# Kernel tuning notes

Hardware: AMD Instinct MI355X
Metric: run time of the kernel (lower is better)

## Reference

```python
import jax, jax.numpy as jnp
import numpy as np

DIM = 64
K = 8
B_TAIL = 3.0
HIDDEN = 64
BATCH = 16384
MIN_BIN_WIDTH = 1e-3
MIN_BIN_HEIGHT = 1e-3
MIN_DERIVATIVE = 1e-3


def setup_inputs() -> dict:
    key = jax.random.key(0)
    ks = jax.random.split(key, 8)
    L = DIM - 1
    out_dim = 3 * K - 1
    def u(k, shape, fan_in):
        b = 1.0 / np.sqrt(fan_in)
        return jax.random.uniform(k, shape, minval=-b, maxval=b, dtype=jnp.float32)
    return {
        "x": jax.random.normal(ks[0], (BATCH, DIM), jnp.float32),
        "init_param": jax.random.uniform(ks[1], (out_dim,), minval=-0.5, maxval=0.5, dtype=jnp.float32),
        # conditioner MLP i (i=1..dim-1) maps x[:, :i] -> 3K-1; stacked with zero-masked inputs
        "W1": u(ks[2], (L, HIDDEN, DIM), DIM),
        "b1": u(ks[3], (L, HIDDEN), DIM),
        "W2": u(ks[4], (L, HIDDEN, HIDDEN), HIDDEN),
        "b2": u(ks[5], (L, HIDDEN), HIDDEN),
        "W3": u(ks[6], (L, out_dim, HIDDEN), HIDDEN),
        "b3": u(ks[7], (L, out_dim), HIDDEN),
    }


def _rqs(inputs, uW, uH, uD, left, right):
    # inputs: [D, B]; uW/uH: [D, B, K]; uD: [D, B, K+1] (already edge-padded)
    num_bins = uW.shape[-1]
    widths = jax.nn.softmax(uW, axis=-1)
    widths = MIN_BIN_WIDTH + (1 - MIN_BIN_WIDTH * num_bins) * widths
    cw = jnp.pad(jnp.cumsum(widths, axis=-1), ((0, 0), (0, 0), (1, 0)))
    cw = (right - left) * cw + left
    cw = cw.at[..., 0].set(left).at[..., -1].set(right)
    widths = cw[..., 1:] - cw[..., :-1]

    derivs = MIN_DERIVATIVE + jax.nn.softplus(uD)

    heights = jax.nn.softmax(uH, axis=-1)
    heights = MIN_BIN_HEIGHT + (1 - MIN_BIN_HEIGHT * num_bins) * heights
    ch = jnp.pad(jnp.cumsum(heights, axis=-1), ((0, 0), (0, 0), (1, 0)))
    ch = (right - left) * ch + left  # bottom=left, top=right (symmetric box)
    ch = ch.at[..., 0].set(left).at[..., -1].set(right)
    heights = ch[..., 1:] - ch[..., :-1]

    # searchsorted: sum(inputs >= bin_edges) - 1, with eps on last edge
    cw_s = cw.at[..., -1].add(1e-6)
    bin_idx = jnp.sum(inputs[..., None] >= cw_s, axis=-1) - 1
    bin_idx = jnp.clip(bin_idx, 0, num_bins - 1)[..., None]
    take = lambda a: jnp.take_along_axis(a, bin_idx, axis=-1)[..., 0]

    in_cw = take(cw)
    in_w = take(widths)
    in_ch = take(ch)
    in_h = take(heights)
    in_delta = take(heights / widths)
    d_k = take(derivs)
    d_k1 = take(derivs[..., 1:])

    theta = (inputs - in_cw) / in_w
    t1mt = theta * (1 - theta)
    numer = in_h * (in_delta * theta**2 + d_k * t1mt)
    denom = in_delta + (d_k + d_k1 - 2 * in_delta) * t1mt
    outputs = in_ch + numer / denom
    dnum = in_delta**2 * (d_k1 * theta**2 + 2 * in_delta * t1mt + d_k * (1 - theta) ** 2)
    logabsdet = jnp.log(dnum) - 2 * jnp.log(denom)
    return outputs, logabsdet


def _unconstrained_rqs(inputs, uW, uH, uD, tail_bound):
    inside = (inputs >= -tail_bound) & (inputs <= tail_bound)
    const = float(np.log(np.exp(1 - MIN_DERIVATIVE) - 1))
    uD = jnp.pad(uD, ((0, 0), (0, 0), (1, 1)), constant_values=const)
    x_in = jnp.clip(inputs, -tail_bound, tail_bound)
    out, ld = _rqs(x_in, uW, uH, uD, -tail_bound, tail_bound)
    return jnp.where(inside, out, inputs), jnp.where(inside, ld, 0.0)


def reference(x, init_param, W1, b1, W2, b2, W3, b3):
    Bsz = x.shape[0]
    L = DIM - 1
    # row l of mask keeps x[:, :l+1], zeroes the rest -> identical to per-layer x[:, :i]
    mask = jnp.tril(jnp.ones((L, DIM), x.dtype))
    xm = x[None, :, :] * mask[:, None, :]                         # [L, B, D]
    h = jnp.tanh(jnp.einsum('lbd,lhd->lbh', xm, W1) + b1[:, None, :])
    h = jnp.tanh(jnp.einsum('lbh,lgh->lbg', h, W2) + b2[:, None, :])
    out = jnp.einsum('lbh,loh->lbo', h, W3) + b3[:, None, :]      # [L, B, 3K-1]
    params = jnp.concatenate(
        [jnp.broadcast_to(init_param, (1, Bsz, 3 * K - 1)), out], axis=0)  # [D, B, 3K-1]
    W = 2 * B_TAIL * jax.nn.softmax(params[..., :K], axis=-1)
    H = 2 * B_TAIL * jax.nn.softmax(params[..., K:2 * K], axis=-1)
    Dp = jax.nn.softplus(params[..., 2 * K:])
    z_t, ld = _unconstrained_rqs(x.T, W, H, Dp, B_TAIL)           # [D, B]
    return z_t.T, ld.sum(axis=0)
```

## Files before the change

### kernel.cpp

```cpp
#include <hip/hip_runtime.h>

#define BATCH 16384
#define LAYERS 63
#define BM 128
#define XS 72
#define BLOB_BYTES 21504
#define LDS_OFF 8192
#define LDS_BYTES 13312

typedef float f4 __attribute__((ext_vector_type(4)));
typedef short s8 __attribute__((ext_vector_type(8)));
typedef unsigned int u4 __attribute__((ext_vector_type(4)));

__device__ __forceinline__ float rcpf(float v) { return __builtin_amdgcn_rcpf(v); }

__device__ __forceinline__ float fast_tanh(float v) {
    float e = __expf(2.f * v);
    return 1.f - 2.f * rcpf(e + 1.f);
}
__device__ __forceinline__ float softplus_f(float v) {
    return fmaxf(v, 0.f) + __logf(1.f + __expf(-fabsf(v)));
}
__device__ __forceinline__ unsigned short f2bf(float f) {
    unsigned int u = __float_as_uint(f);
    u += 0x7fffu + ((u >> 16) & 1u);
    return (unsigned short)(u >> 16);
}
#if __has_builtin(__builtin_amdgcn_cvt_pk_bf16_f32)
__device__ __forceinline__ unsigned pk2(float a, float b) {
    auto r = __builtin_amdgcn_cvt_pk_bf16_f32(a, b);
    return __builtin_bit_cast(unsigned, r);
}
#else
__device__ __forceinline__ unsigned pk2(float a, float b) {
    return (unsigned)f2bf(a) | ((unsigned)f2bf(b) << 16);
}
#endif
__device__ __forceinline__ unsigned long long pack4(float a, float b, float c, float d) {
    return (unsigned long long)pk2(a, b) | ((unsigned long long)pk2(c, d) << 32);
}

__device__ __forceinline__ void rqs_eval(const float* p, float xv, float& zout, float& ldout) {
    const bool inside = (xv >= -3.f) && (xv <= 3.f);
    const float xi = fminf(fmaxf(xv, -3.f), 3.f);

    float wa[8], ha[8];
    {
        float s = 0.f;
        #pragma unroll
        for (int i = 0; i < 8; i++) { wa[i] = __expf(p[i]); s += wa[i]; }
        float inv = 6.f * rcpf(s);
        #pragma unroll
        for (int i = 0; i < 8; i++) wa[i] *= inv;
        s = 0.f;
        #pragma unroll
        for (int i = 0; i < 8; i++) { wa[i] = __expf(wa[i]); s += wa[i]; }
        inv = 0.992f * rcpf(s);
        #pragma unroll
        for (int i = 0; i < 8; i++) wa[i] = 1e-3f + wa[i] * inv;
    }
    {
        float s = 0.f;
        #pragma unroll
        for (int i = 0; i < 8; i++) { ha[i] = __expf(p[8 + i]); s += ha[i]; }
        float inv = 6.f * rcpf(s);
        #pragma unroll
        for (int i = 0; i < 8; i++) ha[i] *= inv;
        s = 0.f;
        #pragma unroll
        for (int i = 0; i < 8; i++) { ha[i] = __expf(ha[i]); s += ha[i]; }
        inv = 0.992f * rcpf(s);
        #pragma unroll
        for (int i = 0; i < 8; i++) ha[i] = 1e-3f + ha[i] * inv;
    }

    float cw[9], ch[9];
    cw[0] = -3.f; ch[0] = -3.f;
    {
        float cs = 0.f, hs = 0.f;
        #pragma unroll
        for (int k = 1; k < 8; k++) {
            cs += wa[k - 1]; cw[k] = 6.f * cs - 3.f;
            hs += ha[k - 1]; ch[k] = 6.f * hs - 3.f;
        }
    }
    cw[8] = 3.f; ch[8] = 3.f;

    int cnt = 0;
    #pragma unroll
    for (int k = 0; k < 8; k++) cnt += (xi >= cw[k]) ? 1 : 0;
    cnt += (xi >= 3.000001f) ? 1 : 0;
    const int bin = min(max(cnt - 1, 0), 7);

    float in_cw = 0.f, in_w = 1.f, in_ch = 0.f, in_h = 1.f;
    float pd0 = 0.f, pd1 = 0.f;
    #pragma unroll
    for (int k = 0; k < 8; k++)
        if (k == bin) {
            in_cw = cw[k]; in_w = cw[k + 1] - cw[k];
            in_ch = ch[k]; in_h = ch[k + 1] - ch[k];
            if (k >= 1) pd0 = p[15 + k];
            if (k <= 6) pd1 = p[16 + k];
        }
    const float dk  = (bin == 0) ? 1.f : 1e-3f + softplus_f(softplus_f(pd0));
    const float dk1 = (bin == 7) ? 1.f : 1e-3f + softplus_f(softplus_f(pd1));

    const float rw    = rcpf(in_w);
    const float delta = in_h * rw;
    const float th    = (xi - in_cw) * rw;
    const float omt = 1.f - th;
    const float t1  = th * omt;
    const float th2 = th * th;
    const float numer = in_h * (delta * th2 + dk * t1);
    const float denom = delta + (dk + dk1 - 2.f * delta) * t1;
    const float outv  = in_ch + numer * rcpf(denom);
    const float dnum  = delta * delta * (dk1 * th2 + 2.f * delta * t1 + dk * omt * omt);
    const float ldv = __logf(dnum) - 2.f * __logf(denom);

    zout  = inside ? outv : xv;
    ldout = inside ? ldv : 0.f;
}

__global__ __launch_bounds__(256) void prep_kernel(
    const float* __restrict__ W1, const float* __restrict__ W2, const float* __restrict__ W3,
    const float* __restrict__ b1, const float* __restrict__ b2, const float* __restrict__ b3,
    unsigned char* __restrict__ blobG)
{
    const int tid = threadIdx.x;
    const int l = blockIdx.x;
    unsigned char* gb = blobG + (size_t)l * BLOB_BYTES;
    for (int e = tid; e < 1024; e += 256) {
        int m = e >> 9, r = (e >> 3) & 63, j = e & 7;
        const float* src = (m ? W2 : W1) + (size_t)l * 4096 + r * 64 + j * 8;
        unsigned long long lo = pack4(src[0], src[1], src[2], src[3]);
        unsigned long long hi = pack4(src[4], src[5], src[6], src[7]);
        unsigned long long* dst = (unsigned long long*)(gb + m * 8192 + r * 128 + ((j ^ (r & 7)) << 4));
        dst[0] = lo; dst[1] = hi;
    }
    if (tid < 256) {
        int r = tid >> 3, j = tid & 7;
        unsigned long long lo = 0ull, hi = 0ull;
        if (r < 23) {
            const float* src = W3 + (size_t)l * 1472 + r * 64 + j * 8;
            lo = pack4(src[0], src[1], src[2], src[3]);
            hi = pack4(src[4], src[5], src[6], src[7]);
        }
        unsigned long long* dst = (unsigned long long*)(gb + 16384 + r * 128 + ((j ^ (r & 7)) << 4));
        dst[0] = lo; dst[1] = hi;
    }
    if (tid < 64)        *(float*)(gb + 20480 + tid * 4)         = b1[l * 64 + tid];
    else if (tid < 128)  *(float*)(gb + 20736 + (tid - 64) * 4)  = b2[l * 64 + tid - 64];
    else if (tid < 160)  *(float*)(gb + 20992 + (tid - 128) * 4) = (tid - 128 < 23) ? b3[l * 23 + tid - 128] : 0.f;
    else                 { int e = tid - 160; if (e < 96) *(float*)(gb + 21120 + e * 4) = 0.f; }
}

__global__ __launch_bounds__(256, 5) void mlp_rqs_kernel(
    const float* __restrict__ x, const float* __restrict__ init_param,
    const unsigned char* __restrict__ blobG,
    float* __restrict__ z, float* __restrict__ ld)
{
    const int l = blockIdx.y;
    const int tid = threadIdx.x;

    if (l == LAYERS) {
        if (tid < 128) {
            const int row = blockIdx.x * 128 + tid;
            float p[23];
            #pragma unroll
            for (int j = 0; j < 23; j++) p[j] = init_param[j];
            float zv, lv;
            rqs_eval(p, x[(size_t)row * 64], zv, lv);
            z[(size_t)row * 64] = zv;
            unsafeAtomicAdd(ld + row, lv);
        }
        return;
    }

    const int keff = l + 1;
    const int b0 = blockIdx.x * BM;
    const int ln = tid & 63, wv = tid >> 6;
    const int c = ln & 15, q = ln >> 4;
    const int mbase = wv * 32;
    const int c7 = c & 7;

    __shared__ __align__(16) unsigned char blob[LDS_BYTES];
    __shared__ __align__(16) unsigned short Hs[BM * XS];

    unsigned short* W2s = (unsigned short*)blob;
    unsigned short* W3s = (unsigned short*)(blob + 8192);
    const float* b1s = (const float*)(blob + 12288);
    const float* b2s = (const float*)(blob + 12544);
    const float* b3s = (const float*)(blob + 12800);
    float* PsF = (float*)Hs;

    const unsigned char* gblob = blobG + (size_t)l * BLOB_BYTES;

    for (int t = wv; t < 13; t += 4)
        __builtin_amdgcn_global_load_lds(
            (const __attribute__((address_space(1))) void*)(gblob + LDS_OFF + t * 1024 + ln * 16),
            (__attribute__((address_space(3))) void*)(blob + t * 1024 + ln * 16), 16, 0, 0);

    const int ks1 = (keff + 31) >> 5;

    s8 aw1[2][4];
    #pragma unroll
    for (int mt = 0; mt < 4; mt++)
        aw1[0][mt] = *(const s8*)(gblob + (mt * 16 + c) * 128 + ((q ^ c7) << 4));
    if (ks1 == 2) {
        #pragma unroll
        for (int mt = 0; mt < 4; mt++)
            aw1[1][mt] = *(const s8*)(gblob + (mt * 16 + c) * 128 + (((4 + q) ^ c7) << 4));
    }

    u4 B0u, B1u, B2u{}, B3u{};
    {
        const float* xr = x + (size_t)(b0 + mbase + c) * 64 + q * 8;
        f4 v0a = *(const f4*)xr,            v0b = *(const f4*)(xr + 4);
        f4 v1a = *(const f4*)(xr + 1024),   v1b = *(const f4*)(xr + 1028);
        B0u = u4{pk2(v0a[0], v0a[1]), pk2(v0a[2], v0a[3]), pk2(v0b[0], v0b[1]), pk2(v0b[2], v0b[3])};
        B1u = u4{pk2(v1a[0], v1a[1]), pk2(v1a[2], v1a[3]), pk2(v1b[0], v1b[1]), pk2(v1b[2], v1b[3])};
        if (ks1 == 2) {
            f4 w0a = *(const f4*)(xr + 32),        w0b = *(const f4*)(xr + 36);
            f4 w1a = *(const f4*)(xr + 1024 + 32), w1b = *(const f4*)(xr + 1024 + 36);
            B2u = u4{pk2(w0a[0], w0a[1]), pk2(w0a[2], w0a[3]), pk2(w0b[0], w0b[1]), pk2(w0b[2], w0b[3])};
            B3u = u4{pk2(w1a[0], w1a[1]), pk2(w1a[2], w1a[3]), pk2(w1b[0], w1b[1]), pk2(w1b[2], w1b[3])};
        }
        const int n = keff - ((ks1 - 1) * 32 + q * 8);
        unsigned mk[4];
        #pragma unroll
        for (int i = 0; i < 4; i++) {
            int m = n - 2 * i;
            mk[i] = (m >= 2) ? 0xFFFFFFFFu : ((m == 1) ? 0xFFFFu : 0u);
        }
        if (ks1 == 2) {
            #pragma unroll
            for (int i = 0; i < 4; i++) { B2u[i] &= mk[i]; B3u[i] &= mk[i]; }
        } else {
            #pragma unroll
            for (int i = 0; i < 4; i++) { B0u[i] &= mk[i]; B1u[i] &= mk[i]; }
        }
    }
    const float xv = x[(size_t)(b0 + (tid & 127)) * 64 + keff];

    __syncthreads();

    {
        f4 acc[4][2];
        #pragma unroll
        for (int mt = 0; mt < 4; mt++) {
            f4 bv = *(const f4*)&b1s[mt * 16 + q * 4];
            acc[mt][0] = bv; acc[mt][1] = bv;
        }
        {
            s8 bx0 = __builtin_bit_cast(s8, B0u), bx1 = __builtin_bit_cast(s8, B1u);
            #pragma unroll
            for (int mt = 0; mt < 4; mt++) {
                acc[mt][0] = __builtin_amdgcn_mfma_f32_16x16x32_bf16(aw1[0][mt], bx0, acc[mt][0], 0, 0, 0);
                acc[mt][1] = __builtin_amdgcn_mfma_f32_16x16x32_bf16(aw1[0][mt], bx1, acc[mt][1], 0, 0, 0);
            }
        }
        if (ks1 == 2) {
            s8 bx0 = __builtin_bit_cast(s8, B2u), bx1 = __builtin_bit_cast(s8, B3u);
            #pragma unroll
            for (int mt = 0; mt < 4; mt++) {
                acc[mt][0] = __builtin_amdgcn_mfma_f32_16x16x32_bf16(aw1[1][mt], bx0, acc[mt][0], 0, 0, 0);
                acc[mt][1] = __builtin_amdgcn_mfma_f32_16x16x32_bf16(aw1[1][mt], bx1, acc[mt][1], 0, 0, 0);
            }
        }
        #pragma unroll
        for (int mt = 0; mt < 4; mt++)
            #pragma unroll
            for (int nt = 0; nt < 2; nt++) {
                f4 a = acc[mt][nt];
                unsigned long long w = (unsigned long long)pk2(fast_tanh(a[0]), fast_tanh(a[1]))
                    | ((unsigned long long)pk2(fast_tanh(a[2]), fast_tanh(a[3])) << 32);
                *(unsigned long long*)&Hs[(mbase + nt * 16 + c) * XS + mt * 16 + q * 4] = w;
            }
    }

    {
        f4 acc[4][2];
        #pragma unroll
        for (int mt = 0; mt < 4; mt++) {
            f4 bv = *(const f4*)&b2s[mt * 16 + q * 4];
            acc[mt][0] = bv; acc[mt][1] = bv;
        }
        #pragma unroll
        for (int ks = 0; ks < 2; ks++) {
            s8 bh0 = *(const s8*)&Hs[(mbase + c) * XS + ks * 32 + q * 8];
            s8 bh1 = *(const s8*)&Hs[(mbase + 16 + c) * XS + ks * 32 + q * 8];
            const int sb = ((ks * 4 + q) ^ c7) * 8;
            #pragma unroll
            for (int mt = 0; mt < 4; mt++) {
                s8 aw = *(const s8*)&W2s[(mt * 16 + c) * 64 + sb];
                acc[mt][0] = __builtin_amdgcn_mfma_f32_16x16x32_bf16(aw, bh0, acc[mt][0], 0, 0, 0);
                acc[mt][1] = __builtin_amdgcn_mfma_f32_16x16x32_bf16(aw, bh1, acc[mt][1], 0, 0, 0);
            }
        }
        #pragma unroll
        for (int mt = 0; mt < 4; mt++)
            #pragma unroll
            for (int nt = 0; nt < 2; nt++) {
                f4 a = acc[mt][nt];
                unsigned long long w = (unsigned long long)pk2(fast_tanh(a[0]), fast_tanh(a[1]))
                    | ((unsigned long long)pk2(fast_tanh(a[2]), fast_tanh(a[3])) << 32);
                *(unsigned long long*)&Hs[(mbase + nt * 16 + c) * XS + mt * 16 + q * 4] = w;
            }
    }

    {
        f4 acc3[2][2];
        #pragma unroll
        for (int mt = 0; mt < 2; mt++) {
            f4 bv = *(const f4*)&b3s[mt * 16 + q * 4];
            acc3[mt][0] = bv; acc3[mt][1] = bv;
        }
        #pragma unroll
        for (int ks = 0; ks < 2; ks++) {
            s8 bh0 = *(const s8*)&Hs[(mbase + c) * XS + ks * 32 + q * 8];
            s8 bh1 = *(const s8*)&Hs[(mbase + 16 + c) * XS + ks * 32 + q * 8];
            const int sb = ((ks * 4 + q) ^ c7) * 8;
            #pragma unroll
            for (int mt = 0; mt < 2; mt++) {
                s8 aw = *(const s8*)&W3s[(mt * 16 + c) * 64 + sb];
                acc3[mt][0] = __builtin_amdgcn_mfma_f32_16x16x32_bf16(aw, bh0, acc3[mt][0], 0, 0, 0);
                acc3[mt][1] = __builtin_amdgcn_mfma_f32_16x16x32_bf16(aw, bh1, acc3[mt][1], 0, 0, 0);
            }
        }
        #pragma unroll
        for (int mt = 0; mt < 2; mt++)
            #pragma unroll
            for (int nt = 0; nt < 2; nt++)
                *(f4*)&PsF[(mbase + nt * 16 + c) * 36 + mt * 16 + q * 4] = acc3[mt][nt];
    }
    __syncthreads();

    if (tid < BM) {
        float p[23];
        #pragma unroll
        for (int j = 0; j < 23; j++) p[j] = PsF[tid * 36 + j];
        float zv, lv;
        rqs_eval(p, xv, zv, lv);
        z[(size_t)(b0 + tid) * 64 + keff] = zv;
        unsafeAtomicAdd(ld + b0 + tid, lv);
    }
}

extern "C" void kernel_launch(void* const* d_in, const int* in_sizes, int n_in,
                              void* d_out, int out_size, void* d_ws, size_t ws_size,
                              hipStream_t stream)
{
    const float* x  = (const float*)d_in[0];
    const float* ip = (const float*)d_in[1];
    const float* W1 = (const float*)d_in[2];
    const float* b1 = (const float*)d_in[3];
    const float* W2 = (const float*)d_in[4];
    const float* b2 = (const float*)d_in[5];
    const float* W3 = (const float*)d_in[6];
    const float* b3 = (const float*)d_in[7];

    float* z  = (float*)d_out;
    float* ld = z + (size_t)BATCH * 64;

    unsigned char* blobG = (unsigned char*)d_ws;

    prep_kernel<<<LAYERS, 256, 0, stream>>>(W1, W2, W3, b1, b2, b3, blobG);
    hipMemsetAsync(ld, 0, BATCH * sizeof(float), stream);
    mlp_rqs_kernel<<<dim3(BATCH / BM, LAYERS + 1), 256, 0, stream>>>(
        x, ip, blobG, z, ld);
}
```

Before: 134.0 us.

## Shrink LDS footprint with swizzled H buffer and register-held W3 to raise occupancy

Replaces the padded H staging buffer (stride 72) with an unpadded XOR-swizzled layout and swizzles the parameter output buffer as well, so bank conflicts stay low without padding. W3 is no longer staged through LDS; each wave loads its fragments directly from global memory into registers. The blob layout is repacked so only W2 and the biases go to LDS, and launch bounds rise from 5 to 6 blocks per CU. The aim is more resident blocks per CU, traded against extra global loads for W3 and more register pressure.

```diff
diff --git a/kernel.cpp b/kernel.cpp
--- a/kernel.cpp
+++ b/kernel.cpp
@@ -3,10 +3,8 @@
 #define BATCH 16384
 #define LAYERS 63
 #define BM 128
-#define XS 72
 #define BLOB_BYTES 21504
-#define LDS_OFF 8192
-#define LDS_BYTES 13312
+#define LDSA_BYTES 9216
 
 typedef float f4 __attribute__((ext_vector_type(4)));
 typedef short s8 __attribute__((ext_vector_type(8)));
@@ -145,16 +143,16 @@
             lo = pack4(src[0], src[1], src[2], src[3]);
             hi = pack4(src[4], src[5], src[6], src[7]);
         }
-        unsigned long long* dst = (unsigned long long*)(gb + 16384 + r * 128 + ((j ^ (r & 7)) << 4));
+        unsigned long long* dst = (unsigned long long*)(gb + 17408 + r * 128 + ((j ^ (r & 7)) << 4));
         dst[0] = lo; dst[1] = hi;
     }
-    if (tid < 64)        *(float*)(gb + 20480 + tid * 4)         = b1[l * 64 + tid];
-    else if (tid < 128)  *(float*)(gb + 20736 + (tid - 64) * 4)  = b2[l * 64 + tid - 64];
-    else if (tid < 160)  *(float*)(gb + 20992 + (tid - 128) * 4) = (tid - 128 < 23) ? b3[l * 23 + tid - 128] : 0.f;
-    else                 { int e = tid - 160; if (e < 96) *(float*)(gb + 21120 + e * 4) = 0.f; }
-}
-
-__global__ __launch_bounds__(256, 5) void mlp_rqs_kernel(
+    if (tid < 64)        *(float*)(gb + 16384 + tid * 4)         = b1[l * 64 + tid];
+    else if (tid < 128)  *(float*)(gb + 16640 + (tid - 64) * 4)  = b2[l * 64 + tid - 64];
+    else if (tid < 160)  *(float*)(gb + 16896 + (tid - 128) * 4) = (tid - 128 < 23) ? b3[l * 23 + tid - 128] : 0.f;
+    else                 *(float*)(gb + 17024 + (tid - 160) * 4) = 0.f;
+}
+
+__global__ __launch_bounds__(256, 6) void mlp_rqs_kernel(
     const float* __restrict__ x, const float* __restrict__ init_param,
     const unsigned char* __restrict__ blobG,
     float* __restrict__ z, float* __restrict__ ld)
@@ -183,22 +181,21 @@
     const int mbase = wv * 32;
     const int c7 = c & 7;
 
-    __shared__ __align__(16) unsigned char blob[LDS_BYTES];
-    __shared__ __align__(16) unsigned short Hs[BM * XS];
-
-    unsigned short* W2s = (unsigned short*)blob;
-    unsigned short* W3s = (unsigned short*)(blob + 8192);
-    const float* b1s = (const float*)(blob + 12288);
-    const float* b2s = (const float*)(blob + 12544);
-    const float* b3s = (const float*)(blob + 12800);
+    __shared__ __align__(16) unsigned char ldsA[LDSA_BYTES];
+    __shared__ __align__(16) unsigned short Hs[BM * 64];
+
+    unsigned short* W2s = (unsigned short*)ldsA;
+    const float* b1s = (const float*)(ldsA + 8192);
+    const float* b2s = (const float*)(ldsA + 8448);
+    const float* b3s = (const float*)(ldsA + 8704);
     float* PsF = (float*)Hs;
 
     const unsigned char* gblob = blobG + (size_t)l * BLOB_BYTES;
 
-    for (int t = wv; t < 13; t += 4)
+    for (int t = wv; t < 9; t += 4)
         __builtin_amdgcn_global_load_lds(
-            (const __attribute__((address_space(1))) void*)(gblob + LDS_OFF + t * 1024 + ln * 16),
-            (__attribute__((address_space(3))) void*)(blob + t * 1024 + ln * 16), 16, 0, 0);
+            (const __attribute__((address_space(1))) void*)(gblob + 8192 + t * 1024 + ln * 16),
+            (__attribute__((address_space(3))) void*)(ldsA + t * 1024 + ln * 16), 16, 0, 0);
 
     const int ks1 = (keff + 31) >> 5;
 
@@ -242,6 +239,9 @@
     }
     const float xv = x[(size_t)(b0 + (tid & 127)) * 64 + keff];
 
+    const int row0 = (mbase + c) * 64, row1 = (mbase + 16 + c) * 64;
+    const int qoff = (q & 1) << 2, qhalf = q >> 1;
+
     __syncthreads();
 
     {
@@ -274,9 +274,17 @@
                 f4 a = acc[mt][nt];
                 unsigned long long w = (unsigned long long)pk2(fast_tanh(a[0]), fast_tanh(a[1]))
                     | ((unsigned long long)pk2(fast_tanh(a[2]), fast_tanh(a[3])) << 32);
-                *(unsigned long long*)&Hs[(mbase + nt * 16 + c) * XS + mt * 16 + q * 4] = w;
-            }
-    }
+                *(unsigned long long*)&Hs[(nt ? row1 : row0)
+                    + ((((mt << 1) + qhalf) ^ c7) << 3) + qoff] = w;
+            }
+    }
+
+    s8 aw3[2][2];
+    #pragma unroll
+    for (int ks = 0; ks < 2; ks++)
+        #pragma unroll
+        for (int mt = 0; mt < 2; mt++)
+            aw3[ks][mt] = *(const s8*)(gblob + 17408 + (mt * 16 + c) * 128 + (((ks * 4 + q) ^ c7) << 4));
 
     {
         f4 acc[4][2];
@@ -287,8 +295,8 @@
         }
         #pragma unroll
         for (int ks = 0; ks < 2; ks++) {
-            s8 bh0 = *(const s8*)&Hs[(mbase + c) * XS + ks * 32 + q * 8];
-            s8 bh1 = *(const s8*)&Hs[(mbase + 16 + c) * XS + ks * 32 + q * 8];
+            s8 bh0 = *(const s8*)&Hs[row0 + (((ks * 4 + q) ^ c7) << 3)];
+            s8 bh1 = *(const s8*)&Hs[row1 + (((ks * 4 + q) ^ c7) << 3)];
             const int sb = ((ks * 4 + q) ^ c7) * 8;
             #pragma unroll
             for (int mt = 0; mt < 4; mt++) {
@@ -304,7 +312,8 @@
                 f4 a = acc[mt][nt];
                 unsigned long long w = (unsigned long long)pk2(fast_tanh(a[0]), fast_tanh(a[1]))
                     | ((unsigned long long)pk2(fast_tanh(a[2]), fast_tanh(a[3])) << 32);
-                *(unsigned long long*)&Hs[(mbase + nt * 16 + c) * XS + mt * 16 + q * 4] = w;
+                *(unsigned long long*)&Hs[(nt ? row1 : row0)
+                    + ((((mt << 1) + qhalf) ^ c7) << 3) + qoff] = w;
             }
     }
 
@@ -317,28 +326,30 @@
         }
         #pragma unroll
         for (int ks = 0; ks < 2; ks++) {
-            s8 bh0 = *(const s8*)&Hs[(mbase + c) * XS + ks * 32 + q * 8];
-            s8 bh1 = *(const s8*)&Hs[(mbase + 16 + c) * XS + ks * 32 + q * 8];
-            const int sb = ((ks * 4 + q) ^ c7) * 8;
+            s8 bh0 = *(const s8*)&Hs[row0 + (((ks * 4 + q) ^ c7) << 3)];
+            s8 bh1 = *(const s8*)&Hs[row1 + (((ks * 4 + q) ^ c7) << 3)];
             #pragma unroll
             for (int mt = 0; mt < 2; mt++) {
-                s8 aw = *(const s8*)&W3s[(mt * 16 + c) * 64 + sb];
-                acc3[mt][0] = __builtin_amdgcn_mfma_f32_16x16x32_bf16(aw, bh0, acc3[mt][0], 0, 0, 0);
-                acc3[mt][1] = __builtin_amdgcn_mfma_f32_16x16x32_bf16(aw, bh1, acc3[mt][1], 0, 0, 0);
+                acc3[mt][0] = __builtin_amdgcn_mfma_f32_16x16x32_bf16(aw3[ks][mt], bh0, acc3[mt][0], 0, 0, 0);
+                acc3[mt][1] = __builtin_amdgcn_mfma_f32_16x16x32_bf16(aw3[ks][mt], bh1, acc3[mt][1], 0, 0, 0);
             }
         }
         #pragma unroll
         for (int mt = 0; mt < 2; mt++)
             #pragma unroll
             for (int nt = 0; nt < 2; nt++)
-                *(f4*)&PsF[(mbase + nt * 16 + c) * 36 + mt * 16 + q * 4] = acc3[mt][nt];
+                *(f4*)&PsF[(mbase + nt * 16 + c) * 32 + (((mt * 4 + q) ^ c7) << 2)] = acc3[mt][nt];
     }
     __syncthreads();
 
     if (tid < BM) {
+        const int t7 = tid & 7;
+        f4 pr[6];
+        #pragma unroll
+        for (int i = 0; i < 6; i++) pr[i] = *(const f4*)&PsF[tid * 32 + ((i ^ t7) << 2)];
         float p[23];
         #pragma unroll
-        for (int j = 0; j < 23; j++) p[j] = PsF[tid * 36 + j];
+        for (int j = 0; j < 23; j++) p[j] = pr[j >> 2][j & 3];
         float zv, lv;
         rqs_eval(p, xv, zv, lv);
         z[(size_t)(b0 + tid) * 64 + keff] = zv;
```

After: 138.0 us. 1.03x slower.
